# Optimization experiments

Hardware: AMD Instinct MI355X
Metric: run time of the kernel (lower is better)

Reference implementation:

```python
import jax, jax.numpy as jnp
import numpy as np

DIM = 768
HEADS = 12
HEAD_DIM = DIM // HEADS
SCALE = HEAD_DIM ** -0.5


def setup_inputs() -> dict:
    key = jax.random.key(0)
    ks = jax.random.split(key, 9)
    B, N, M, C = 4, 1024, 1024, DIM
    std = C ** -0.5
    return {
        "q": jax.random.normal(ks[0], (B, N, C), jnp.float32),
        "k": jax.random.normal(ks[1], (B, M, C), jnp.float32),
        "v": jax.random.normal(ks[2], (B, M, C), jnp.float32),
        "mask": jax.random.uniform(ks[3], (B, N, M), jnp.float32),
        "Wq": jax.random.normal(ks[4], (C, C), jnp.float32) * std,
        "Wk": jax.random.normal(ks[5], (C, C), jnp.float32) * std,
        "Wv": jax.random.normal(ks[6], (C, C), jnp.float32) * std,
        "Wp": jax.random.normal(ks[7], (C, C), jnp.float32) * std,
        "bp": jax.random.normal(ks[8], (C,), jnp.float32) * 0.01,
    }


def reference(q, k, v, mask, Wq, Wk, Wv, Wp, bp):
    B, N, C = q.shape
    M = k.shape[1]
    H, D = HEADS, HEAD_DIM
    qh = (q @ Wq).reshape(B, N, H, D)
    kh = (k @ Wk).reshape(B, M, H, D)
    vh = (v @ Wv).reshape(B, M, H, D)
    attn = jnp.einsum('bnhd,bmhd->bhnm', qh, kh) * SCALE
    attn = jax.nn.softmax(attn, axis=-1)
    # post-softmax multiplicative mask, broadcast over heads
    attn = attn * mask[:, None, :, :]
    x = jnp.einsum('bhnm,bmhd->bnhd', attn, vh).reshape(B, N, C)
    return x @ Wp + bp
```

## Files before the change

kernel.cpp:

```cpp
#include <hip/hip_runtime.h>

typedef __bf16 bf16x8 __attribute__((ext_vector_type(8)));
typedef float f32x4 __attribute__((ext_vector_type(4)));

__device__ __forceinline__ unsigned short f2bf(float f) {
  union { float f; unsigned u; } x; x.f = f;
  unsigned r = x.u + 0x7FFFu + ((x.u >> 16) & 1u);
  return (unsigned short)(r >> 16);
}

__device__ __forceinline__ void gload_lds16(const void* g, void* l) {
  __builtin_amdgcn_global_load_lds(
      (const __attribute__((address_space(1))) unsigned int*)g,
      (__attribute__((address_space(3))) unsigned int*)l, 16, 0, 0);
}

__device__ __forceinline__ f32x4 mfma16(bf16x8 a, bf16x8 b, f32x4 c) {
  return __builtin_amdgcn_mfma_f32_16x16x32_bf16(a, b, c, 0, 0, 0);
}

__global__ __launch_bounds__(256) void conv_qkv(const float* __restrict__ q,
                                                const float* __restrict__ k,
                                                const float* __restrict__ v,
                                                unsigned short* __restrict__ dst) {
  const float* src = (blockIdx.y == 0) ? q : (blockIdx.y == 1 ? k : v);
  size_t i = ((size_t)blockIdx.x * 256 + threadIdx.x) * 4;
  float4 f = *(const float4*)(src + i);
  ushort4 u;
  u.x = f2bf(f.x); u.y = f2bf(f.y); u.z = f2bf(f.z); u.w = f2bf(f.w);
  *(ushort4*)(dst + (size_t)blockIdx.y * (4096u * 768u) + i) = u;
}

__global__ __launch_bounds__(256) void conv_w(const float* __restrict__ W0,
                                              const float* __restrict__ W1,
                                              const float* __restrict__ W2,
                                              const float* __restrict__ W3,
                                              unsigned short* __restrict__ Wt) {
  __shared__ float tile[32][33];
  const float* W = (blockIdx.z == 0) ? W0 : (blockIdx.z == 1) ? W1
                   : (blockIdx.z == 2) ? W2 : W3;
  int tx = threadIdx.x, ty = threadIdx.y;
  int n0 = blockIdx.x * 32, k0 = blockIdx.y * 32;
#pragma unroll
  for (int i = 0; i < 4; ++i)
    tile[ty * 4 + i][tx] = W[(size_t)(k0 + ty * 4 + i) * 768 + n0 + tx];
  __syncthreads();
  unsigned short* o = Wt + (size_t)blockIdx.z * 768 * 768;
#pragma unroll
  for (int i = 0; i < 4; ++i)
    o[(size_t)(n0 + ty * 4 + i) * 768 + k0 + tx] = f2bf(tile[tx][ty * 4 + i]);
}

__device__ __forceinline__ void gemm_core(const unsigned short* __restrict__ A,
                                          const unsigned short* __restrict__ B,
                                          unsigned short* As, unsigned short* Bs,
                                          int m0, int n0, int wm, int wn,
                                          int t, int g, int c16,
                                          f32x4 (&acc)[4][4]) {
  for (int k0 = 0; k0 < 768; k0 += 64) {
    if (k0) __syncthreads();
#pragma unroll
    for (int i = 0; i < 4; ++i) {
      int fc = i * 256 + t;
      int r = fc >> 3, c = (fc & 7) ^ (r & 7);
      gload_lds16(A + (size_t)(m0 + r) * 768 + k0 + c * 8, (char*)As + fc * 16);
      gload_lds16(B + (size_t)(n0 + r) * 768 + k0 + c * 8, (char*)Bs + fc * 16);
    }
    __syncthreads();
#pragma unroll
    for (int kk = 0; kk < 2; ++kk) {
      const int ch = kk * 4 + g;
      bf16x8 a[4], b[4];
#pragma unroll
      for (int mi = 0; mi < 4; ++mi) {
        int r = wm + mi * 16 + c16;
        a[mi] = *(const bf16x8*)((char*)As + r * 128 + ((ch ^ (r & 7)) << 4));
      }
#pragma unroll
      for (int ni = 0; ni < 4; ++ni) {
        int r = wn + ni * 16 + c16;
        b[ni] = *(const bf16x8*)((char*)Bs + r * 128 + ((ch ^ (r & 7)) << 4));
      }
#pragma unroll
      for (int mi = 0; mi < 4; ++mi)
#pragma unroll
        for (int ni = 0; ni < 4; ++ni)
          acc[mi][ni] = mfma16(a[mi], b[ni], acc[mi][ni]);
    }
  }
}

__global__ __launch_bounds__(256) void gemm_qkv(const unsigned short* __restrict__ Abase,
                                                const unsigned short* __restrict__ Wt,
                                                unsigned short* __restrict__ Hq,
                                                unsigned short* __restrict__ Hk,
                                                unsigned short* __restrict__ Hvt) {
  __shared__ unsigned short As[128 * 64], Bs[128 * 64];
  const int z = blockIdx.z;
  const unsigned short* A = Abase + (size_t)z * 4096 * 768;
  const unsigned short* B = Wt + (size_t)z * 768 * 768;
  const int t = threadIdx.x, l = t & 63, wid = t >> 6;
  const int g = l >> 4, c16 = l & 15;
  const int m0 = blockIdx.y * 128, n0 = blockIdx.x * 128;
  const int wm = (wid >> 1) * 64, wn = (wid & 1) * 64;
  f32x4 acc[4][4] = {};
  gemm_core(A, B, As, Bs, m0, n0, wm, wn, t, g, c16, acc);
  if (z < 2) {
    unsigned short* C = (z == 0) ? Hq : Hk;
#pragma unroll
    for (int mi = 0; mi < 4; ++mi)
#pragma unroll
      for (int ni = 0; ni < 4; ++ni) {
        int col = n0 + wn + ni * 16 + c16;
        int row = m0 + wm + mi * 16 + g * 4;
#pragma unroll
        for (int j = 0; j < 4; ++j)
          C[(size_t)(row + j) * 768 + col] = f2bf(acc[mi][ni][j]);
      }
  } else {
#pragma unroll
    for (int mi = 0; mi < 4; ++mi) {
      int rowbase = m0 + wm + mi * 16;
      int bb = rowbase >> 10;
      int mloc = (rowbase & 1023) + g * 4;
#pragma unroll
      for (int ni = 0; ni < 4; ++ni) {
        int col = n0 + wn + ni * 16 + c16;
        ushort4 u;
        u.x = f2bf(acc[mi][ni][0]); u.y = f2bf(acc[mi][ni][1]);
        u.z = f2bf(acc[mi][ni][2]); u.w = f2bf(acc[mi][ni][3]);
        *(ushort4*)(Hvt + (((size_t)(bb * 768 + col)) << 10) + mloc) = u;
      }
    }
  }
}

__global__ __launch_bounds__(256) void attn(const unsigned short* __restrict__ qh,
                                            const unsigned short* __restrict__ kh,
                                            const unsigned short* __restrict__ vhT,
                                            const float* __restrict__ mask,
                                            unsigned short* __restrict__ xb) {
  __shared__ unsigned short Qs[64 * 64], Ks[2][64 * 64], Vts[2][64 * 64], Ps[4 * 16 * 64];
  const int qt = blockIdx.x, h = blockIdx.y, b = blockIdx.z;
  const int t = threadIdx.x, l = t & 63, wid = t >> 6;
  const int g = l >> 4, c16 = l & 15;
#pragma unroll
  for (int i = 0; i < 2; ++i) {
    int fc = i * 256 + t;
    int r = fc >> 3, c = (fc & 7) ^ (r & 7);
    gload_lds16(qh + (size_t)(b * 1024 + qt * 64 + r) * 768 + h * 64 + c * 8,
                (char*)Qs + fc * 16);
    gload_lds16(kh + (size_t)(b * 1024 + r) * 768 + h * 64 + c * 8,
                (char*)Ks[0] + fc * 16);
    gload_lds16(vhT + ((size_t)(b * 768 + h * 64 + r)) * 1024 + c * 8,
                (char*)Vts[0] + fc * 16);
  }
  asm volatile("s_waitcnt vmcnt(0)" ::: "memory");
  __syncthreads();

  f32x4 o[4] = {};
  float lsum[4] = {0.f, 0.f, 0.f, 0.f};
  const float sc = 0.125f * 1.44269504088896341f;
  unsigned short* Pw = Ps + wid * (16 * 64);
  for (int kv = 0; kv < 16; ++kv) {
    const int cur = kv & 1;
    if (kv + 1 < 16) {
#pragma unroll
      for (int i = 0; i < 2; ++i) {
        int fc = i * 256 + t;
        int r = fc >> 3, c = (fc & 7) ^ (r & 7);
        gload_lds16(kh + (size_t)(b * 1024 + (kv + 1) * 64 + r) * 768 + h * 64 + c * 8,
                    (char*)Ks[cur ^ 1] + fc * 16);
        gload_lds16(vhT + ((size_t)(b * 768 + h * 64 + r)) * 1024 + (kv + 1) * 64 + c * 8,
                    (char*)Vts[cur ^ 1] + fc * 16);
      }
    }
    float mreg[4][4];
    const float* mbase = mask + ((size_t)(b * 1024 + qt * 64 + wid * 16 + g * 4)) * 1024 + kv * 64;
#pragma unroll
    for (int ni = 0; ni < 4; ++ni)
#pragma unroll
      for (int j = 0; j < 4; ++j)
        mreg[ni][j] = mbase[(size_t)j * 1024 + ni * 16 + c16];
    f32x4 p[4] = {};
#pragma unroll
    for (int kk = 0; kk < 2; ++kk) {
      const int ch = kk * 4 + g;
      int rq = wid * 16 + c16;
      bf16x8 aq = *(const bf16x8*)((char*)Qs + rq * 128 + ((ch ^ (rq & 7)) << 4));
#pragma unroll
      for (int ni = 0; ni < 4; ++ni) {
        int r = ni * 16 + c16;
        bf16x8 bk = *(const bf16x8*)((char*)Ks[cur] + r * 128 + ((ch ^ (r & 7)) << 4));
        p[ni] = mfma16(aq, bk, p[ni]);
      }
    }
#pragma unroll
    for (int j = 0; j < 4; ++j) {
      float e0 = exp2f(p[0][j] * sc);
      float e1 = exp2f(p[1][j] * sc);
      float e2 = exp2f(p[2][j] * sc);
      float e3 = exp2f(p[3][j] * sc);
      p[0][j] = e0; p[1][j] = e1; p[2][j] = e2; p[3][j] = e3;
      float s = e0 + e1 + e2 + e3;
      s += __shfl_xor(s, 1);
      s += __shfl_xor(s, 2);
      s += __shfl_xor(s, 4);
      s += __shfl_xor(s, 8);
      lsum[j] += s;
    }
#pragma unroll
    for (int ni = 0; ni < 4; ++ni)
#pragma unroll
      for (int j = 0; j < 4; ++j) {
        float pv = p[ni][j] * mreg[ni][j];
        int row = g * 4 + j, col = ni * 16 + c16;
        *(unsigned short*)((char*)Pw + row * 128 +
                           (((col >> 3) ^ (row & 7)) << 4) + ((col & 7) << 1)) = f2bf(pv);
      }
    asm volatile("s_waitcnt lgkmcnt(0)" ::: "memory");
#pragma unroll
    for (int kk = 0; kk < 2; ++kk) {
      const int ch = kk * 4 + g;
      int rp = c16;
      bf16x8 ap = *(const bf16x8*)((char*)Pw + rp * 128 + ((ch ^ (rp & 7)) << 4));
#pragma unroll
      for (int ni = 0; ni < 4; ++ni) {
        int r = ni * 16 + c16;
        bf16x8 bv = *(const bf16x8*)((char*)Vts[cur] + r * 128 + ((ch ^ (r & 7)) << 4));
        o[ni] = mfma16(ap, bv, o[ni]);
      }
    }
    asm volatile("s_waitcnt vmcnt(0)" ::: "memory");
    __syncthreads();
  }
#pragma unroll
  for (int ni = 0; ni < 4; ++ni) {
    int col = h * 64 + ni * 16 + c16;
    int row = qt * 64 + wid * 16 + g * 4;
#pragma unroll
    for (int j = 0; j < 4; ++j)
      xb[((size_t)(b * 1024) + row + j) * 768 + col] = f2bf(o[ni][j] / lsum[j]);
  }
}

__global__ __launch_bounds__(256) void gemm_proj(const unsigned short* __restrict__ A,
                                                 const unsigned short* __restrict__ B,
                                                 const float* __restrict__ bias,
                                                 float* __restrict__ C) {
  __shared__ unsigned short As[128 * 64], Bs[128 * 64];
  const int t = threadIdx.x, l = t & 63, wid = t >> 6;
  const int g = l >> 4, c16 = l & 15;
  const int m0 = blockIdx.y * 128, n0 = blockIdx.x * 128;
  const int wm = (wid >> 1) * 64, wn = (wid & 1) * 64;
  f32x4 acc[4][4] = {};
  gemm_core(A, B, As, Bs, m0, n0, wm, wn, t, g, c16, acc);
#pragma unroll
  for (int mi = 0; mi < 4; ++mi)
#pragma unroll
    for (int ni = 0; ni < 4; ++ni) {
      int col = n0 + wn + ni * 16 + c16;
      int row = m0 + wm + mi * 16 + g * 4;
      float bv = bias[col];
#pragma unroll
      for (int j = 0; j < 4; ++j)
        C[(size_t)(row + j) * 768 + col] = acc[mi][ni][j] + bv;
    }
}

extern "C" void kernel_launch(void* const* d_in, const int* in_sizes, int n_in,
                              void* d_out, int out_size, void* d_ws, size_t ws_size,
                              hipStream_t stream) {
  const float* q    = (const float*)d_in[0];
  const float* k    = (const float*)d_in[1];
  const float* v    = (const float*)d_in[2];
  const float* mask = (const float*)d_in[3];
  const float* Wq   = (const float*)d_in[4];
  const float* Wk   = (const float*)d_in[5];
  const float* Wv   = (const float*)d_in[6];
  const float* Wp   = (const float*)d_in[7];
  const float* bp   = (const float*)d_in[8];
  float* out = (float*)d_out;

  const size_t MN = (size_t)4096 * 768;
  const size_t WW = (size_t)768 * 768;
  unsigned short* qkv_bf = (unsigned short*)d_ws;
  unsigned short* wt     = qkv_bf + 3 * MN;
  unsigned short* heads  = wt + 4 * WW;
  unsigned short* xb     = heads + 3 * MN;

  conv_qkv<<<dim3(3072, 3), 256, 0, stream>>>(q, k, v, qkv_bf);
  conv_w<<<dim3(24, 24, 4), dim3(32, 8), 0, stream>>>(Wq, Wk, Wv, Wp, wt);
  gemm_qkv<<<dim3(6, 32, 3), 256, 0, stream>>>(qkv_bf, wt, heads, heads + MN, heads + 2 * MN);
  attn<<<dim3(16, 12, 4), 256, 0, stream>>>(heads, heads + MN, heads + 2 * MN, mask, xb);
  gemm_proj<<<dim3(6, 32), 256, 0, stream>>>(xb, wt + 3 * WW, bp, out);
}
```

Before: 112.0 us.

## Double-buffer GEMM tiles, shrink M tile, keep Q in registers, defer softmax sum

The GEMM core now double-buffers its A/B LDS tiles so the next K-slice loads while the current one computes. The M tile shrinks from 128 to 64, which doubles the grid to improve CU occupancy on the 4096x768 GEMMs. The LDS swizzle changes to XOR with (row>>1). In attention, Q fragments are loaded directly into registers instead of LDS, and the per-tile cross-lane softmax-sum shuffles are deferred to a single reduction at the end. Attention also advances pointers incrementally and drops the per-iteration vmcnt wait. The risks are smaller per-block reuse in the GEMMs and a possible race from removing the vmcnt wait before the barrier.

```diff
diff --git a/kernel.cpp b/kernel.cpp
--- a/kernel.cpp
+++ b/kernel.cpp
@@ -53,40 +53,56 @@
 
 __device__ __forceinline__ void gemm_core(const unsigned short* __restrict__ A,
                                           const unsigned short* __restrict__ B,
-                                          unsigned short* As, unsigned short* Bs,
+                                          unsigned short (*As)[64 * 64],
+                                          unsigned short (*Bs)[128 * 64],
                                           int m0, int n0, int wm, int wn,
                                           int t, int g, int c16,
-                                          f32x4 (&acc)[4][4]) {
-  for (int k0 = 0; k0 < 768; k0 += 64) {
-    if (k0) __syncthreads();
+                                          f32x4 (&acc)[2][4]) {
+  auto stageA = [&](unsigned short* dst, int k0) {
+#pragma unroll
+    for (int i = 0; i < 2; ++i) {
+      int fc = i * 256 + t, r = fc >> 3, c = (fc & 7) ^ ((r >> 1) & 7);
+      gload_lds16(A + (size_t)(m0 + r) * 768 + k0 + c * 8, (char*)dst + fc * 16);
+    }
+  };
+  auto stageB = [&](unsigned short* dst, int k0) {
 #pragma unroll
     for (int i = 0; i < 4; ++i) {
-      int fc = i * 256 + t;
-      int r = fc >> 3, c = (fc & 7) ^ (r & 7);
-      gload_lds16(A + (size_t)(m0 + r) * 768 + k0 + c * 8, (char*)As + fc * 16);
-      gload_lds16(B + (size_t)(n0 + r) * 768 + k0 + c * 8, (char*)Bs + fc * 16);
-    }
-    __syncthreads();
+      int fc = i * 256 + t, r = fc >> 3, c = (fc & 7) ^ ((r >> 1) & 7);
+      gload_lds16(B + (size_t)(n0 + r) * 768 + k0 + c * 8, (char*)dst + fc * 16);
+    }
+  };
+  stageA(As[0], 0);
+  stageB(Bs[0], 0);
+  asm volatile("s_waitcnt vmcnt(0)" ::: "memory");
+  __syncthreads();
+  for (int s = 0; s < 12; ++s) {
+    const int cur = s & 1;
+    if (s < 11) {
+      stageA(As[cur ^ 1], (s + 1) * 64);
+      stageB(Bs[cur ^ 1], (s + 1) * 64);
+    }
 #pragma unroll
     for (int kk = 0; kk < 2; ++kk) {
       const int ch = kk * 4 + g;
-      bf16x8 a[4], b[4];
-#pragma unroll
-      for (int mi = 0; mi < 4; ++mi) {
+      bf16x8 a[2], bw[4];
+#pragma unroll
+      for (int mi = 0; mi < 2; ++mi) {
         int r = wm + mi * 16 + c16;
-        a[mi] = *(const bf16x8*)((char*)As + r * 128 + ((ch ^ (r & 7)) << 4));
+        a[mi] = *(const bf16x8*)((char*)As[cur] + r * 128 + (((ch ^ (r >> 1)) & 7) << 4));
       }
 #pragma unroll
       for (int ni = 0; ni < 4; ++ni) {
         int r = wn + ni * 16 + c16;
-        b[ni] = *(const bf16x8*)((char*)Bs + r * 128 + ((ch ^ (r & 7)) << 4));
-      }
-#pragma unroll
-      for (int mi = 0; mi < 4; ++mi)
+        bw[ni] = *(const bf16x8*)((char*)Bs[cur] + r * 128 + (((ch ^ (r >> 1)) & 7) << 4));
+      }
+#pragma unroll
+      for (int mi = 0; mi < 2; ++mi)
 #pragma unroll
         for (int ni = 0; ni < 4; ++ni)
-          acc[mi][ni] = mfma16(a[mi], b[ni], acc[mi][ni]);
-    }
+          acc[mi][ni] = mfma16(a[mi], bw[ni], acc[mi][ni]);
+    }
+    __syncthreads();
   }
 }
 
@@ -95,20 +111,20 @@
                                                 unsigned short* __restrict__ Hq,
                                                 unsigned short* __restrict__ Hk,
                                                 unsigned short* __restrict__ Hvt) {
-  __shared__ unsigned short As[128 * 64], Bs[128 * 64];
+  __shared__ unsigned short As[2][64 * 64], Bs[2][128 * 64];
   const int z = blockIdx.z;
   const unsigned short* A = Abase + (size_t)z * 4096 * 768;
   const unsigned short* B = Wt + (size_t)z * 768 * 768;
   const int t = threadIdx.x, l = t & 63, wid = t >> 6;
   const int g = l >> 4, c16 = l & 15;
-  const int m0 = blockIdx.y * 128, n0 = blockIdx.x * 128;
-  const int wm = (wid >> 1) * 64, wn = (wid & 1) * 64;
-  f32x4 acc[4][4] = {};
+  const int m0 = blockIdx.y * 64, n0 = blockIdx.x * 128;
+  const int wm = (wid >> 1) * 32, wn = (wid & 1) * 64;
+  f32x4 acc[2][4] = {};
   gemm_core(A, B, As, Bs, m0, n0, wm, wn, t, g, c16, acc);
   if (z < 2) {
     unsigned short* C = (z == 0) ? Hq : Hk;
 #pragma unroll
-    for (int mi = 0; mi < 4; ++mi)
+    for (int mi = 0; mi < 2; ++mi)
 #pragma unroll
       for (int ni = 0; ni < 4; ++ni) {
         int col = n0 + wn + ni * 16 + c16;
@@ -119,9 +135,9 @@
       }
   } else {
 #pragma unroll
-    for (int mi = 0; mi < 4; ++mi) {
+    for (int mi = 0; mi < 2; ++mi) {
       int rowbase = m0 + wm + mi * 16;
-      int bb = rowbase >> 10;
+      int bat = rowbase >> 10;
       int mloc = (rowbase & 1023) + g * 4;
 #pragma unroll
       for (int ni = 0; ni < 4; ++ni) {
@@ -129,7 +145,7 @@
         ushort4 u;
         u.x = f2bf(acc[mi][ni][0]); u.y = f2bf(acc[mi][ni][1]);
         u.z = f2bf(acc[mi][ni][2]); u.w = f2bf(acc[mi][ni][3]);
-        *(ushort4*)(Hvt + (((size_t)(bb * 768 + col)) << 10) + mloc) = u;
+        *(ushort4*)(Hvt + (((size_t)(bat * 768 + col)) << 10) + mloc) = u;
       }
     }
   }
@@ -140,58 +156,71 @@
                                             const unsigned short* __restrict__ vhT,
                                             const float* __restrict__ mask,
                                             unsigned short* __restrict__ xb) {
-  __shared__ unsigned short Qs[64 * 64], Ks[2][64 * 64], Vts[2][64 * 64], Ps[4 * 16 * 64];
+  __shared__ unsigned short Ks[2][64 * 64], Vts[2][64 * 64], Ps[4 * 16 * 64];
   const int qt = blockIdx.x, h = blockIdx.y, b = blockIdx.z;
   const int t = threadIdx.x, l = t & 63, wid = t >> 6;
   const int g = l >> 4, c16 = l & 15;
-#pragma unroll
-  for (int i = 0; i < 2; ++i) {
-    int fc = i * 256 + t;
-    int r = fc >> 3, c = (fc & 7) ^ (r & 7);
-    gload_lds16(qh + (size_t)(b * 1024 + qt * 64 + r) * 768 + h * 64 + c * 8,
-                (char*)Qs + fc * 16);
-    gload_lds16(kh + (size_t)(b * 1024 + r) * 768 + h * 64 + c * 8,
-                (char*)Ks[0] + fc * 16);
-    gload_lds16(vhT + ((size_t)(b * 768 + h * 64 + r)) * 1024 + c * 8,
-                (char*)Vts[0] + fc * 16);
-  }
+
+  const unsigned short* qp =
+      qh + ((size_t)(b * 1024 + qt * 64 + wid * 16 + c16)) * 768 + h * 64 + g * 8;
+  bf16x8 aq0 = *(const bf16x8*)qp;
+  bf16x8 aq1 = *(const bf16x8*)(qp + 32);
+
+  const int fc0 = t, r0 = fc0 >> 3, c0 = (fc0 & 7) ^ ((r0 >> 1) & 7);
+  const int fc1 = 256 + t, r1 = fc1 >> 3, c1 = (fc1 & 7) ^ ((r1 >> 1) & 7);
+  const unsigned short* kp0 = kh + (size_t)(b * 1024 + r0) * 768 + h * 64 + c0 * 8;
+  const unsigned short* kp1 = kh + (size_t)(b * 1024 + r1) * 768 + h * 64 + c1 * 8;
+  const unsigned short* vp0 = vhT + ((size_t)(b * 768 + h * 64 + r0)) * 1024 + c0 * 8;
+  const unsigned short* vp1 = vhT + ((size_t)(b * 768 + h * 64 + r1)) * 1024 + c1 * 8;
+  gload_lds16(kp0, (char*)Ks[0] + fc0 * 16);
+  gload_lds16(kp1, (char*)Ks[0] + fc1 * 16);
+  gload_lds16(vp0, (char*)Vts[0] + fc0 * 16);
+  gload_lds16(vp1, (char*)Vts[0] + fc1 * 16);
+  kp0 += 64 * 768; kp1 += 64 * 768; vp0 += 64; vp1 += 64;
+
+  const float* mrow0 =
+      mask + ((size_t)(b * 1024 + qt * 64 + wid * 16 + g * 4)) * 1024 + c16;
+  const float* mrow1 = mrow0 + 1024;
+  const float* mrow2 = mrow0 + 2048;
+  const float* mrow3 = mrow0 + 3072;
+
   asm volatile("s_waitcnt vmcnt(0)" ::: "memory");
   __syncthreads();
 
   f32x4 o[4] = {};
-  float lsum[4] = {0.f, 0.f, 0.f, 0.f};
+  float ls[4] = {0.f, 0.f, 0.f, 0.f};
   const float sc = 0.125f * 1.44269504088896341f;
-  unsigned short* Pw = Ps + wid * (16 * 64);
+  char* Pw = (char*)Ps + wid * 2048;
+
   for (int kv = 0; kv < 16; ++kv) {
     const int cur = kv & 1;
-    if (kv + 1 < 16) {
-#pragma unroll
-      for (int i = 0; i < 2; ++i) {
-        int fc = i * 256 + t;
-        int r = fc >> 3, c = (fc & 7) ^ (r & 7);
-        gload_lds16(kh + (size_t)(b * 1024 + (kv + 1) * 64 + r) * 768 + h * 64 + c * 8,
-                    (char*)Ks[cur ^ 1] + fc * 16);
-        gload_lds16(vhT + ((size_t)(b * 768 + h * 64 + r)) * 1024 + (kv + 1) * 64 + c * 8,
-                    (char*)Vts[cur ^ 1] + fc * 16);
-      }
+    if (kv < 15) {
+      char* kd = (char*)Ks[cur ^ 1];
+      char* vd = (char*)Vts[cur ^ 1];
+      gload_lds16(kp0, kd + fc0 * 16);
+      gload_lds16(kp1, kd + fc1 * 16);
+      gload_lds16(vp0, vd + fc0 * 16);
+      gload_lds16(vp1, vd + fc1 * 16);
+      kp0 += 64 * 768; kp1 += 64 * 768; vp0 += 64; vp1 += 64;
     }
     float mreg[4][4];
-    const float* mbase = mask + ((size_t)(b * 1024 + qt * 64 + wid * 16 + g * 4)) * 1024 + kv * 64;
-#pragma unroll
-    for (int ni = 0; ni < 4; ++ni)
-#pragma unroll
-      for (int j = 0; j < 4; ++j)
-        mreg[ni][j] = mbase[(size_t)j * 1024 + ni * 16 + c16];
+#pragma unroll
+    for (int ni = 0; ni < 4; ++ni) {
+      mreg[ni][0] = mrow0[ni * 16];
+      mreg[ni][1] = mrow1[ni * 16];
+      mreg[ni][2] = mrow2[ni * 16];
+      mreg[ni][3] = mrow3[ni * 16];
+    }
+    mrow0 += 64; mrow1 += 64; mrow2 += 64; mrow3 += 64;
     f32x4 p[4] = {};
 #pragma unroll
     for (int kk = 0; kk < 2; ++kk) {
       const int ch = kk * 4 + g;
-      int rq = wid * 16 + c16;
-      bf16x8 aq = *(const bf16x8*)((char*)Qs + rq * 128 + ((ch ^ (rq & 7)) << 4));
+      bf16x8 aq = kk ? aq1 : aq0;
 #pragma unroll
       for (int ni = 0; ni < 4; ++ni) {
         int r = ni * 16 + c16;
-        bf16x8 bk = *(const bf16x8*)((char*)Ks[cur] + r * 128 + ((ch ^ (r & 7)) << 4));
+        bf16x8 bk = *(const bf16x8*)((char*)Ks[cur] + r * 128 + (((ch ^ (r >> 1)) & 7) << 4));
         p[ni] = mfma16(aq, bk, p[ni]);
       }
     }
@@ -202,12 +231,7 @@
       float e2 = exp2f(p[2][j] * sc);
       float e3 = exp2f(p[3][j] * sc);
       p[0][j] = e0; p[1][j] = e1; p[2][j] = e2; p[3][j] = e3;
-      float s = e0 + e1 + e2 + e3;
-      s += __shfl_xor(s, 1);
-      s += __shfl_xor(s, 2);
-      s += __shfl_xor(s, 4);
-      s += __shfl_xor(s, 8);
-      lsum[j] += s;
+      ls[j] += (e0 + e1) + (e2 + e3);
     }
 #pragma unroll
     for (int ni = 0; ni < 4; ++ni)
@@ -215,24 +239,31 @@
       for (int j = 0; j < 4; ++j) {
         float pv = p[ni][j] * mreg[ni][j];
         int row = g * 4 + j, col = ni * 16 + c16;
-        *(unsigned short*)((char*)Pw + row * 128 +
-                           (((col >> 3) ^ (row & 7)) << 4) + ((col & 7) << 1)) = f2bf(pv);
+        *(unsigned short*)(Pw + row * 128 +
+                           ((((col >> 3) ^ (row >> 1)) & 7) << 4) + ((col & 7) << 1)) = f2bf(pv);
       }
     asm volatile("s_waitcnt lgkmcnt(0)" ::: "memory");
 #pragma unroll
     for (int kk = 0; kk < 2; ++kk) {
       const int ch = kk * 4 + g;
-      int rp = c16;
-      bf16x8 ap = *(const bf16x8*)((char*)Pw + rp * 128 + ((ch ^ (rp & 7)) << 4));
+      bf16x8 ap = *(const bf16x8*)(Pw + c16 * 128 + (((ch ^ (c16 >> 1)) & 7) << 4));
 #pragma unroll
       for (int ni = 0; ni < 4; ++ni) {
         int r = ni * 16 + c16;
-        bf16x8 bv = *(const bf16x8*)((char*)Vts[cur] + r * 128 + ((ch ^ (r & 7)) << 4));
+        bf16x8 bv = *(const bf16x8*)((char*)Vts[cur] + r * 128 + (((ch ^ (r >> 1)) & 7) << 4));
         o[ni] = mfma16(ap, bv, o[ni]);
       }
     }
-    asm volatile("s_waitcnt vmcnt(0)" ::: "memory");
     __syncthreads();
+  }
+#pragma unroll
+  for (int j = 0; j < 4; ++j) {
+    float s = ls[j];
+    s += __shfl_xor(s, 1);
+    s += __shfl_xor(s, 2);
+    s += __shfl_xor(s, 4);
+    s += __shfl_xor(s, 8);
+    ls[j] = 1.0f / s;
   }
 #pragma unroll
   for (int ni = 0; ni < 4; ++ni) {
@@ -240,7 +271,7 @@
     int row = qt * 64 + wid * 16 + g * 4;
 #pragma unroll
     for (int j = 0; j < 4; ++j)
-      xb[((size_t)(b * 1024) + row + j) * 768 + col] = f2bf(o[ni][j] / lsum[j]);
+      xb[((size_t)(b * 1024) + row + j) * 768 + col] = f2bf(o[ni][j] * ls[j]);
   }
 }
 
@@ -248,15 +279,15 @@
                                                  const unsigned short* __restrict__ B,
                                                  const float* __restrict__ bias,
                                                  float* __restrict__ C) {
-  __shared__ unsigned short As[128 * 64], Bs[128 * 64];
+  __shared__ unsigned short As[2][64 * 64], Bs[2][128 * 64];
   const int t = threadIdx.x, l = t & 63, wid = t >> 6;
   const int g = l >> 4, c16 = l & 15;
-  const int m0 = blockIdx.y * 128, n0 = blockIdx.x * 128;
-  const int wm = (wid >> 1) * 64, wn = (wid & 1) * 64;
-  f32x4 acc[4][4] = {};
+  const int m0 = blockIdx.y * 64, n0 = blockIdx.x * 128;
+  const int wm = (wid >> 1) * 32, wn = (wid & 1) * 64;
+  f32x4 acc[2][4] = {};
   gemm_core(A, B, As, Bs, m0, n0, wm, wn, t, g, c16, acc);
 #pragma unroll
-  for (int mi = 0; mi < 4; ++mi)
+  for (int mi = 0; mi < 2; ++mi)
 #pragma unroll
     for (int ni = 0; ni < 4; ++ni) {
       int col = n0 + wn + ni * 16 + c16;
@@ -291,7 +322,7 @@
 
   conv_qkv<<<dim3(3072, 3), 256, 0, stream>>>(q, k, v, qkv_bf);
   conv_w<<<dim3(24, 24, 4), dim3(32, 8), 0, stream>>>(Wq, Wk, Wv, Wp, wt);
-  gemm_qkv<<<dim3(6, 32, 3), 256, 0, stream>>>(qkv_bf, wt, heads, heads + MN, heads + 2 * MN);
+  gemm_qkv<<<dim3(6, 64, 3), 256, 0, stream>>>(qkv_bf, wt, heads, heads + MN, heads + 2 * MN);
   attn<<<dim3(16, 12, 4), 256, 0, stream>>>(heads, heads + MN, heads + 2 * MN, mask, xb);
-  gemm_proj<<<dim3(6, 32), 256, 0, stream>>>(xb, wt + 3 * WW, bp, out);
-}
+  gemm_proj<<<dim3(6, 64), 256, 0, stream>>>(xb, wt + 3 * WW, bp, out);
+}
```

After: 102.8 us. 8.2% less time.
